# Optimization experiments

Measured on AMD Instinct MI355X. Metric: run time of the kernel, lower is better.

## Reference

```python
import jax, jax.numpy as jnp
import numpy as np

D_MODEL = 768
N_HEADS = 12
D_K = D_MODEL // N_HEADS

def setup_inputs() -> dict:
    key = jax.random.key(0)
    ks = jax.random.split(key, 9)
    B, S = 4, 2048
    s = 1.0 / np.sqrt(D_MODEL)
    return {
        "x": jax.random.normal(ks[0], (B, S, D_MODEL), dtype=jnp.float32),
        "Wq": jax.random.normal(ks[1], (D_MODEL, D_MODEL), dtype=jnp.float32) * s,
        "bq": jnp.zeros((D_MODEL,), dtype=jnp.float32),
        "Wk": jax.random.normal(ks[2], (D_MODEL, D_MODEL), dtype=jnp.float32) * s,
        "bk": jnp.zeros((D_MODEL,), dtype=jnp.float32),
        "Wv": jax.random.normal(ks[3], (D_MODEL, D_MODEL), dtype=jnp.float32) * s,
        "bv": jnp.zeros((D_MODEL,), dtype=jnp.float32),
        "Wo": jax.random.normal(ks[4], (D_MODEL, D_MODEL), dtype=jnp.float32) * s,
        "bo": jnp.zeros((D_MODEL,), dtype=jnp.float32),
    }

def reference(x, Wq, bq, Wk, bk, Wv, bv, Wo, bo):
    B, S, _ = x.shape
    # projections (nn.Linear: x @ W^T + b; here weights stored as (in, out) so x @ W + b)
    q = x @ Wq + bq
    k = x @ Wk + bk
    v = x @ Wv + bv
    # split heads -> (B, H, S, d_k)
    q = q.reshape(B, S, N_HEADS, D_K).transpose(0, 2, 1, 3)
    k = k.reshape(B, S, N_HEADS, D_K).transpose(0, 2, 1, 3)
    v = v.reshape(B, S, N_HEADS, D_K).transpose(0, 2, 1, 3)
    scores = jnp.einsum('bhqd,bhkd->bhqk', q, k) / jnp.sqrt(jnp.float32(D_K))
    causal = jnp.tril(jnp.ones((S, S), dtype=bool))  # True = keep
    scores = jnp.where(causal, scores, jnp.finfo(scores.dtype).min)
    weights = jax.nn.softmax(scores, axis=-1)  # dropout is identity in eval
    out = jnp.einsum('bhqk,bhkd->bhqd', weights, v)
    out = out.transpose(0, 2, 1, 3).reshape(B, S, D_MODEL)
    return out @ Wo + bo
```

## Files before the change

### kernel.cpp

```cpp
#include <hip/hip_runtime.h>
#include <hip/hip_bf16.h>

#define DM    768
#define HEADS 12
#define DK    64
#define SEQ   2048
#define BATCH 4
#define NE    ((size_t)BATCH * SEQ * DM)
#define KT    12
#define BRICK 8192

typedef short v8s __attribute__((ext_vector_type(8)));
typedef float v4f __attribute__((ext_vector_type(4)));

#define LDS_PTR(p) ((__attribute__((address_space(3))) unsigned int*)(p))
#define GLB_PTR(p) ((const __attribute__((address_space(1))) unsigned int*)(p))

__device__ __forceinline__ unsigned short f2bf(float f) {
    union { float f; unsigned u; } v; v.f = f;
    unsigned r = (v.u + 0x7FFFu + ((v.u >> 16) & 1u)) >> 16;
    return (unsigned short)r;
}
__device__ __forceinline__ unsigned pk2(float a, float b) {
    union { float f; unsigned u; } x, y; x.f = a; y.f = b;
    return (x.u >> 16) | (y.u & 0xFFFF0000u);
}
__device__ __forceinline__ unsigned pk2r(float a, float b) {
    return (unsigned)f2bf(a) | ((unsigned)f2bf(b) << 16);
}
__device__ __forceinline__ float fexp2(float x) {
#if __has_builtin(__builtin_amdgcn_exp2f)
    return __builtin_amdgcn_exp2f(x);
#else
    return __expf(x * 0.69314718056f);
#endif
}

#define QSCALE 0.18033688011112042f

__global__ __launch_bounds__(256)
void cvt_x_kernel(const float* __restrict__ x, unsigned short* __restrict__ xb) {
    const size_t p = ((size_t)blockIdx.x * 256 + threadIdx.x) * 8;
    const int m = (int)(p / DM);
    const int k = (int)(p % DM);
    const float4 a = *(const float4*)(x + p);
    const float4 b = *(const float4*)(x + p + 4);
    v8s o;
    o[0] = (short)f2bf(a.x); o[1] = (short)f2bf(a.y);
    o[2] = (short)f2bf(a.z); o[3] = (short)f2bf(a.w);
    o[4] = (short)f2bf(b.x); o[5] = (short)f2bf(b.y);
    o[6] = (short)f2bf(b.z); o[7] = (short)f2bf(b.w);
    const size_t dst = ((size_t)(m >> 7) * KT + (k >> 6)) * BRICK + (size_t)(m & 127) * 64 + (k & 63);
    *(v8s*)(xb + dst) = o;
}

__global__ __launch_bounds__(256)
void cvt_w_kernel(const float* __restrict__ W0, const float* __restrict__ W1,
                  const float* __restrict__ W2, const float* __restrict__ W3,
                  unsigned short* __restrict__ wt) {
    __shared__ unsigned short T[64][72];
    const int z = blockIdx.z;
    const float* W = (z == 0) ? W0 : (z == 1) ? W1 : (z == 2) ? W2 : W3;
    const float scale = (z == 0) ? QSCALE : 1.0f;
    const int k0 = blockIdx.x * 64, n0 = blockIdx.y * 64;
    const int t = threadIdx.x;
    {
        const int kr = t >> 2;
        const int ns = (t & 3) * 16;
        #pragma unroll
        for (int j = 0; j < 4; ++j) {
            const float4 v = *(const float4*)(W + (size_t)(k0 + kr) * DM + n0 + ns + j * 4);
            T[ns + j * 4 + 0][kr] = f2bf(v.x * scale);
            T[ns + j * 4 + 1][kr] = f2bf(v.y * scale);
            T[ns + j * 4 + 2][kr] = f2bf(v.z * scale);
            T[ns + j * 4 + 3][kr] = f2bf(v.w * scale);
        }
    }
    __syncthreads();
    {
        unsigned short* dst = wt + (size_t)z * DM * DM +
            ((size_t)(n0 >> 7) * KT + (k0 >> 6)) * BRICK + (size_t)(n0 & 64) * 64;
        const int n = t >> 2;
        const int ks = (t & 3) * 16;
        #pragma unroll
        for (int j = 0; j < 2; ++j)
            *(v8s*)(dst + (size_t)n * 64 + ks + j * 8) = *(const v8s*)&T[n][ks + j * 8];
    }
}

__global__ __launch_bounds__(256)
void gemm_qkv_kernel(const unsigned short* __restrict__ xb, const unsigned short* __restrict__ wtbuf,
                     const float* __restrict__ bq, const float* __restrict__ bk,
                     const float* __restrict__ bv,
                     unsigned short* __restrict__ qb, unsigned short* __restrict__ kb,
                     unsigned short* __restrict__ vtb) {
    __shared__ unsigned short smem[32768];
    const int idx = blockIdx.x;
    const int xcd = idx & 7, g = idx >> 3;
    const int mb = xcd + 8 * (g & 7);
    const int yb = g >> 3;
    const int z = yb / 6;
    const int N0 = (yb % 6) * 128;
    const float* bias = (z == 0) ? bq : (z == 1) ? bk : bv;
    const float bscale = (z == 0) ? QSCALE : 1.0f;

    const int t = threadIdx.x;
    const int w = t >> 6, lane = t & 63, quad = lane >> 4, l15 = lane & 15;
    const int wm = w >> 1, wn = w & 1;
    const int M0 = mb * 128;

    const unsigned short* gA = xb + (size_t)mb * (KT * BRICK);
    const unsigned short* gB = wtbuf + (size_t)yb * (KT * BRICK);

    const int r8 = lane >> 3;
    const int c8 = (lane & 7) ^ r8;
    const int goff = r8 * 64 + c8 * 8;
    const int rl = l15 & 7, rh = l15 >> 3;

    v4f acc[4][4];
    #pragma unroll
    for (int i = 0; i < 4; ++i)
        #pragma unroll
        for (int j = 0; j < 4; ++j) acc[i][j] = (v4f){0, 0, 0, 0};

    #pragma unroll
    for (int u = 0; u < 4; ++u) {
        const int win = w * 4 + u;
        __builtin_amdgcn_global_load_lds(GLB_PTR(gA + win * 512 + goff), LDS_PTR(smem + win * 512), 16, 0, 0);
        __builtin_amdgcn_global_load_lds(GLB_PTR(gB + win * 512 + goff), LDS_PTR(smem + 16384 + win * 512), 16, 0, 0);
    }
    __syncthreads();

    for (int kt = 0; kt < KT; ++kt) {
        const int cur = kt & 1;
        if (kt + 1 < KT) {
            const unsigned short* ta = gA + (kt + 1) * BRICK;
            const unsigned short* tb = gB + (kt + 1) * BRICK;
            const int nb = (1 - cur) * 8192;
            #pragma unroll
            for (int u = 0; u < 4; ++u) {
                const int win = w * 4 + u;
                __builtin_amdgcn_global_load_lds(GLB_PTR(ta + win * 512 + goff), LDS_PTR(smem + nb + win * 512), 16, 0, 0);
                __builtin_amdgcn_global_load_lds(GLB_PTR(tb + win * 512 + goff), LDS_PTR(smem + 16384 + nb + win * 512), 16, 0, 0);
            }
        }
        const unsigned short* As = smem + cur * 8192;
        const unsigned short* Bs = smem + 16384 + cur * 8192;
        #pragma unroll
        for (int kc = 0; kc < 2; ++kc) {
            const int cs = ((kc << 2) | quad) ^ rl;
            v8s a[4], b[4];
            #pragma unroll
            for (int i = 0; i < 4; ++i)
                a[i] = *(const v8s*)&As[(wm * 8 + i * 2 + rh) * 512 + rl * 64 + cs * 8];
            #pragma unroll
            for (int j = 0; j < 4; ++j)
                b[j] = *(const v8s*)&Bs[(wn * 8 + j * 2 + rh) * 512 + rl * 64 + cs * 8];
            #pragma unroll
            for (int i = 0; i < 4; ++i)
                #pragma unroll
                for (int j = 0; j < 4; ++j)
                    acc[i][j] = __builtin_amdgcn_mfma_f32_16x16x32_bf16(a[i], b[j], acc[i][j], 0, 0, 0);
        }
        __syncthreads();
    }

    const int b_ = M0 >> 11;
    const int sidx0 = M0 & 2047;
    const int h0 = N0 >> 6;

    if (z < 2) {
        unsigned short* outp = (z == 0) ? qb : kb;
        #pragma unroll
        for (int j = 0; j < 4; ++j) {
            const int n = N0 + wn * 64 + j * 16 + l15;
            const int h = n >> 6, d = n & 63;
            const float bv_ = bias[n] * bscale;
            #pragma unroll
            for (int i = 0; i < 4; ++i)
                #pragma unroll
                for (int r = 0; r < 4; ++r) {
                    const int sidx = sidx0 + wm * 64 + i * 16 + quad * 4 + r;
                    outp[(((size_t)(b_ * HEADS + h) * SEQ + sidx) << 6) + d] = f2bf(acc[i][j][r] + bv_);
                }
        }
    } else {
        unsigned short* Ts = smem;
        #pragma unroll
        for (int p = 0; p < 2; ++p) {
            __syncthreads();
            if (wm == p) {
                #pragma unroll
                for (int j = 0; j < 4; ++j) {
                    const int dloc = wn * 64 + j * 16 + l15;
                    const float bv_ = bias[N0 + dloc];
                    #pragma unroll
                    for (int i = 0; i < 4; ++i)
                        #pragma unroll
                        for (int r = 0; r < 4; ++r)
                            Ts[dloc * 72 + i * 16 + quad * 4 + r] = f2bf(acc[i][j][r] + bv_);
                }
            }
            __syncthreads();
            const int dloc = t >> 1, ms = (t & 1) * 32;
            const int h = h0 + (dloc >> 6), d = dloc & 63;
            unsigned short* dst = vtb + (((size_t)(b_ * HEADS + h) * DK + d) << 11) + sidx0 + p * 64 + ms;
            #pragma unroll
            for (int jj = 0; jj < 4; ++jj)
                *(v8s*)(dst + jj * 8) = *(const v8s*)&Ts[dloc * 72 + ms + jj * 8];
        }
    }
}

__global__ __launch_bounds__(256)
void gemm_out_kernel(const unsigned short* __restrict__ ob, const unsigned short* __restrict__ wto,
                     const float* __restrict__ bias, float* __restrict__ out) {
    __shared__ unsigned short smem[32768];
    const int idx = blockIdx.x;
    const int xcd = idx & 7, g = idx >> 3;
    const int mb = xcd + 8 * (g & 7);
    const int nb = g >> 3;
    const int t = threadIdx.x;
    const int w = t >> 6, lane = t & 63, quad = lane >> 4, l15 = lane & 15;
    const int wm = w >> 1, wn = w & 1;
    const int M0 = mb * 128;
    const int N0 = nb * 128;

    const unsigned short* gA = ob + (size_t)mb * (KT * BRICK);
    const unsigned short* gB = wto + (size_t)nb * (KT * BRICK);

    const int r8 = lane >> 3;
    const int c8 = (lane & 7) ^ r8;
    const int goff = r8 * 64 + c8 * 8;
    const int rl = l15 & 7, rh = l15 >> 3;

    v4f acc[4][4];
    #pragma unroll
    for (int i = 0; i < 4; ++i)
        #pragma unroll
        for (int j = 0; j < 4; ++j) acc[i][j] = (v4f){0, 0, 0, 0};

    #pragma unroll
    for (int u = 0; u < 4; ++u) {
        const int win = w * 4 + u;
        __builtin_amdgcn_global_load_lds(GLB_PTR(gA + win * 512 + goff), LDS_PTR(smem + win * 512), 16, 0, 0);
        __builtin_amdgcn_global_load_lds(GLB_PTR(gB + win * 512 + goff), LDS_PTR(smem + 16384 + win * 512), 16, 0, 0);
    }
    __syncthreads();

    for (int kt = 0; kt < KT; ++kt) {
        const int cur = kt & 1;
        if (kt + 1 < KT) {
            const unsigned short* ta = gA + (kt + 1) * BRICK;
            const unsigned short* tb = gB + (kt + 1) * BRICK;
            const int nxt = (1 - cur) * 8192;
            #pragma unroll
            for (int u = 0; u < 4; ++u) {
                const int win = w * 4 + u;
                __builtin_amdgcn_global_load_lds(GLB_PTR(ta + win * 512 + goff), LDS_PTR(smem + nxt + win * 512), 16, 0, 0);
                __builtin_amdgcn_global_load_lds(GLB_PTR(tb + win * 512 + goff), LDS_PTR(smem + 16384 + nxt + win * 512), 16, 0, 0);
            }
        }
        const unsigned short* As = smem + cur * 8192;
        const unsigned short* Bs = smem + 16384 + cur * 8192;
        #pragma unroll
        for (int kc = 0; kc < 2; ++kc) {
            const int cs = ((kc << 2) | quad) ^ rl;
            v8s a[4], b[4];
            #pragma unroll
            for (int i = 0; i < 4; ++i)
                a[i] = *(const v8s*)&As[(wm * 8 + i * 2 + rh) * 512 + rl * 64 + cs * 8];
            #pragma unroll
            for (int j = 0; j < 4; ++j)
                b[j] = *(const v8s*)&Bs[(wn * 8 + j * 2 + rh) * 512 + rl * 64 + cs * 8];
            #pragma unroll
            for (int i = 0; i < 4; ++i)
                #pragma unroll
                for (int j = 0; j < 4; ++j)
                    acc[i][j] = __builtin_amdgcn_mfma_f32_16x16x32_bf16(a[i], b[j], acc[i][j], 0, 0, 0);
        }
        __syncthreads();
    }

    #pragma unroll
    for (int j = 0; j < 4; ++j) {
        const int n = N0 + wn * 64 + j * 16 + l15;
        const float bv_ = bias[n];
        #pragma unroll
        for (int i = 0; i < 4; ++i)
            #pragma unroll
            for (int r = 0; r < 4; ++r) {
                const int m = M0 + wm * 64 + i * 16 + quad * 4 + r;
                out[(size_t)m * DM + n] = acc[i][j][r] + bv_;
            }
    }
}

__global__ __launch_bounds__(256, 3)
void attn_kernel(const unsigned short* __restrict__ Q, const unsigned short* __restrict__ K,
                 const unsigned short* __restrict__ VT, unsigned short* __restrict__ O) {
    __shared__ unsigned short Kb[2][64][72];
    __shared__ unsigned short Vb[2][64][72];
    __shared__ unsigned short Ps[4][16][72];
    const int t = threadIdx.x;
    const int w = t >> 6, lane = t & 63, quad = lane >> 4, l15 = lane & 15;

    const int idx = blockIdx.x;
    const int xcd = idx & 7;
    const int j   = idx >> 3;
    const int bh  = xcd + 8 * (j >> 4);
    const int s   = j & 15;
    const int sA  = s, sB = 31 - s;
    const int q0A = sA * 64, q0B = sB * 64;
    const int nkt = sB + 1;
    const size_t kvbase = (size_t)bh * SEQ * DK;

    v8s qfA[2], qfB[2];
    #pragma unroll
    for (int c = 0; c < 2; ++c) {
        qfA[c] = *(const v8s*)(Q + kvbase + (size_t)(q0A + w * 16 + l15) * DK + c * 32 + quad * 8);
        qfB[c] = *(const v8s*)(Q + kvbase + (size_t)(q0B + w * 16 + l15) * DK + c * 32 + quad * 8);
    }

    v4f oA[4], oB[4];
    #pragma unroll
    for (int nf = 0; nf < 4; ++nf) { oA[nf] = (v4f){0,0,0,0}; oB[nf] = (v4f){0,0,0,0}; }
    float lsA = 0.f, lsB = 0.f;

    const int srow = t >> 3;
    const int scol = (t & 7) * 8;

    v8s kr0 = *(const v8s*)(K  + kvbase + (size_t)srow * DK + scol);
    v8s kr1 = *(const v8s*)(K  + kvbase + (size_t)(srow + 32) * DK + scol);
    v8s vr0 = *(const v8s*)(VT + kvbase + ((size_t)srow << 11) + scol);
    v8s vr1 = *(const v8s*)(VT + kvbase + ((size_t)(srow + 32) << 11) + scol);
    *(v8s*)&Kb[0][srow][scol]      = kr0;
    *(v8s*)&Kb[0][srow + 32][scol] = kr1;
    *(v8s*)&Vb[0][srow][scol]      = vr0;
    *(v8s*)&Vb[0][srow + 32][scol] = vr1;
    __syncthreads();

    const int qA = q0A + w * 16 + l15;
    const int qB = q0B + w * 16 + l15;

    for (int kt = 0; kt < nkt; ++kt) {
        const int k0 = kt * 64;
        const int cur = kt & 1;
        if (kt + 1 < nkt) {
            const int kn = k0 + 64;
            kr0 = *(const v8s*)(K  + kvbase + (size_t)(kn + srow) * DK + scol);
            kr1 = *(const v8s*)(K  + kvbase + (size_t)(kn + srow + 32) * DK + scol);
            vr0 = *(const v8s*)(VT + kvbase + ((size_t)srow << 11) + kn + scol);
            vr1 = *(const v8s*)(VT + kvbase + ((size_t)(srow + 32) << 11) + kn + scol);
        }

        const bool actA = (kt <= sA);

        v4f scB[4], scA[4];
        #pragma unroll
        for (int s4 = 0; s4 < 4; ++s4) { scB[s4] = (v4f){0,0,0,0}; scA[s4] = (v4f){0,0,0,0}; }
        #pragma unroll
        for (int c = 0; c < 2; ++c)
            #pragma unroll
            for (int s4 = 0; s4 < 4; ++s4) {
                const v8s kf = *(const v8s*)&Kb[cur][s4 * 16 + l15][c * 32 + quad * 8];
                scB[s4] = __builtin_amdgcn_mfma_f32_16x16x32_bf16(kf, qfB[c], scB[s4], 0, 0, 0);
                if (actA)
                    scA[s4] = __builtin_amdgcn_mfma_f32_16x16x32_bf16(kf, qfA[c], scA[s4], 0, 0, 0);
            }

        {
            const bool msk = (kt == nkt - 1);
            #pragma unroll
            for (int s4 = 0; s4 < 4; ++s4) {
                float p[4];
                #pragma unroll
                for (int r = 0; r < 4; ++r) {
                    const int key = k0 + s4 * 16 + quad * 4 + r;
                    const float e = fexp2(scB[s4][r]);
                    p[r] = (!msk || key <= qB) ? e : 0.f;
                    lsB += p[r];
                }
                uint2 pkv; pkv.x = pk2(p[0], p[1]); pkv.y = pk2(p[2], p[3]);
                *(uint2*)&Ps[w][l15][s4 * 16 + quad * 4] = pkv;
            }
            #pragma unroll
            for (int kc = 0; kc < 2; ++kc) {
                const v8s pf = *(const v8s*)&Ps[w][l15][kc * 32 + quad * 8];
                #pragma unroll
                for (int nf = 0; nf < 4; ++nf) {
                    const v8s vf = *(const v8s*)&Vb[cur][nf * 16 + l15][kc * 32 + quad * 8];
                    oB[nf] = __builtin_amdgcn_mfma_f32_16x16x32_bf16(vf, pf, oB[nf], 0, 0, 0);
                }
            }
        }

        if (actA) {
            const bool msk = (kt == sA);
            #pragma unroll
            for (int s4 = 0; s4 < 4; ++s4) {
                float p[4];
                #pragma unroll
                for (int r = 0; r < 4; ++r) {
                    const int key = k0 + s4 * 16 + quad * 4 + r;
                    const float e = fexp2(scA[s4][r]);
                    p[r] = (!msk || key <= qA) ? e : 0.f;
                    lsA += p[r];
                }
                uint2 pkv; pkv.x = pk2(p[0], p[1]); pkv.y = pk2(p[2], p[3]);
                *(uint2*)&Ps[w][l15][s4 * 16 + quad * 4] = pkv;
            }
            #pragma unroll
            for (int kc = 0; kc < 2; ++kc) {
                const v8s pf = *(const v8s*)&Ps[w][l15][kc * 32 + quad * 8];
                #pragma unroll
                for (int nf = 0; nf < 4; ++nf) {
                    const v8s vf = *(const v8s*)&Vb[cur][nf * 16 + l15][kc * 32 + quad * 8];
                    oA[nf] = __builtin_amdgcn_mfma_f32_16x16x32_bf16(vf, pf, oA[nf], 0, 0, 0);
                }
            }
        }

        if (kt + 1 < nkt) {
            const int nxt = 1 - cur;
            *(v8s*)&Kb[nxt][srow][scol]      = kr0;
            *(v8s*)&Kb[nxt][srow + 32][scol] = kr1;
            *(v8s*)&Vb[nxt][srow][scol]      = vr0;
            *(v8s*)&Vb[nxt][srow + 32][scol] = vr1;
        }
        __syncthreads();
    }

    lsA += __shfl_xor(lsA, 16); lsA += __shfl_xor(lsA, 32);
    lsB += __shfl_xor(lsB, 16); lsB += __shfl_xor(lsB, 32);
    const float invA = 1.f / lsA, invB = 1.f / lsB;

    const int b = bh / HEADS, h = bh % HEADS;
    const size_t brA = ((size_t)(b * 16 + (q0A >> 7)) * KT + h) * BRICK;
    const size_t brB = ((size_t)(b * 16 + (q0B >> 7)) * KT + h) * BRICK;
    const int rowlA = (q0A & 127) + w * 16 + l15;
    const int rowlB = (q0B & 127) + w * 16 + l15;
    #pragma unroll
    for (int nf = 0; nf < 4; ++nf) {
        uint2 a2, b2;
        a2.x = pk2r(oA[nf][0] * invA, oA[nf][1] * invA);
        a2.y = pk2r(oA[nf][2] * invA, oA[nf][3] * invA);
        b2.x = pk2r(oB[nf][0] * invB, oB[nf][1] * invB);
        b2.y = pk2r(oB[nf][2] * invB, oB[nf][3] * invB);
        *(uint2*)(O + brA + (size_t)rowlA * 64 + nf * 16 + quad * 4) = a2;
        *(uint2*)(O + brB + (size_t)rowlB * 64 + nf * 16 + quad * 4) = b2;
    }
}

extern "C" void kernel_launch(void* const* d_in, const int* in_sizes, int n_in,
                              void* d_out, int out_size, void* d_ws, size_t ws_size,
                              hipStream_t stream) {
    const float* x  = (const float*)d_in[0];
    const float* Wq = (const float*)d_in[1];
    const float* bq = (const float*)d_in[2];
    const float* Wk = (const float*)d_in[3];
    const float* bk = (const float*)d_in[4];
    const float* Wv = (const float*)d_in[5];
    const float* bv = (const float*)d_in[6];
    const float* Wo = (const float*)d_in[7];
    const float* bo = (const float*)d_in[8];
    float* out = (float*)d_out;

    unsigned short* xb  = (unsigned short*)d_ws;
    unsigned short* qb  = xb  + NE;
    unsigned short* kb  = qb  + NE;
    unsigned short* vtb = kb  + NE;
    unsigned short* wt  = vtb + NE;
    unsigned short* ob  = xb;

    cvt_x_kernel<<<dim3(NE / (8 * 256)), 256, 0, stream>>>(x, xb);
    cvt_w_kernel<<<dim3(12, 12, 4), 256, 0, stream>>>(Wq, Wk, Wv, Wo, wt);
    gemm_qkv_kernel<<<dim3(1152), 256, 0, stream>>>(xb, wt, bq, bk, bv, qb, kb, vtb);
    attn_kernel<<<dim3(768), 256, 0, stream>>>(qb, kb, vtb, ob);
    gemm_out_kernel<<<dim3(384), 256, 0, stream>>>(ob, wt + (size_t)3 * DM * DM, bo, out);
}
```

Before: 212.9 us.

## Keep softmax probabilities in registers and feed PV via 16x16x16 MFMA

Removes the per-wave LDS round trip for the probability tile. The score MFMA output layout (4 consecutive keys per lane) is fed directly as the B operand of a 16x16x16 bf16 MFMA, so the exp'd scores are packed in registers with v_perm. The causal mask is also split into an unmasked fast path for non-diagonal tiles, and the A and B query blocks now share each V fragment load. The trade-off is twice as many, smaller MFMAs for PV, which have lower per-instruction throughput, plus extra live registers for pA/pB.

```diff
diff --git a/kernel.cpp b/kernel.cpp
--- a/kernel.cpp
+++ b/kernel.cpp
@@ -11,6 +11,7 @@
 #define BRICK 8192
 
 typedef short v8s __attribute__((ext_vector_type(8)));
+typedef short v4s __attribute__((ext_vector_type(4)));
 typedef float v4f __attribute__((ext_vector_type(4)));
 
 #define LDS_PTR(p) ((__attribute__((address_space(3))) unsigned int*)(p))
@@ -20,10 +21,6 @@
     union { float f; unsigned u; } v; v.f = f;
     unsigned r = (v.u + 0x7FFFu + ((v.u >> 16) & 1u)) >> 16;
     return (unsigned short)r;
-}
-__device__ __forceinline__ unsigned pk2(float a, float b) {
-    union { float f; unsigned u; } x, y; x.f = a; y.f = b;
-    return (x.u >> 16) | (y.u & 0xFFFF0000u);
 }
 __device__ __forceinline__ unsigned pk2r(float a, float b) {
     return (unsigned)f2bf(a) | ((unsigned)f2bf(b) << 16);
@@ -33,6 +30,18 @@
     return __builtin_amdgcn_exp2f(x);
 #else
     return __expf(x * 0.69314718056f);
+#endif
+}
+__device__ __forceinline__ unsigned permpk(float a, float b) {
+    union { float f; unsigned u; } x, y; x.f = a; y.f = b;
+    return __builtin_amdgcn_perm(y.u, x.u, 0x07060302u);
+}
+__device__ __forceinline__ v4f mfma16x16x16(v4s a, v4s b, v4f c) {
+#if __has_builtin(__builtin_amdgcn_mfma_f32_16x16x16bf16_1k)
+    return __builtin_amdgcn_mfma_f32_16x16x16bf16_1k(a, b, c, 0, 0, 0);
+#else
+    asm volatile("v_mfma_f32_16x16x16_bf16 %0, %1, %2, %0" : "+v"(c) : "v"(a), "v"(b));
+    return c;
 #endif
 }
 
@@ -301,7 +310,6 @@
                  const unsigned short* __restrict__ VT, unsigned short* __restrict__ O) {
     __shared__ unsigned short Kb[2][64][72];
     __shared__ unsigned short Vb[2][64][72];
-    __shared__ unsigned short Ps[4][16][72];
     const int t = threadIdx.x;
     const int w = t >> 6, lane = t & 63, quad = lane >> 4, l15 = lane & 15;
 
@@ -324,7 +332,7 @@
 
     v4f oA[4], oB[4];
     #pragma unroll
-    for (int nf = 0; nf < 4; ++nf) { oA[nf] = (v4f){0,0,0,0}; oB[nf] = (v4f){0,0,0,0}; }
+    for (int df = 0; df < 4; ++df) { oA[df] = (v4f){0,0,0,0}; oB[df] = (v4f){0,0,0,0}; }
     float lsA = 0.f, lsB = 0.f;
 
     const int srow = t >> 3;
@@ -342,6 +350,7 @@
 
     const int qA = q0A + w * 16 + l15;
     const int qB = q0B + w * 16 + l15;
+    const int kqbase = quad * 4;
 
     for (int kt = 0; kt < nkt; ++kt) {
         const int k0 = kt * 64;
@@ -369,55 +378,63 @@
                     scA[s4] = __builtin_amdgcn_mfma_f32_16x16x32_bf16(kf, qfA[c], scA[s4], 0, 0, 0);
             }
 
-        {
-            const bool msk = (kt == nkt - 1);
+        uint2 pB[4], pA[4];
+        if (kt < nkt - 1) {
+            #pragma unroll
+            for (int s4 = 0; s4 < 4; ++s4) {
+                const float p0 = fexp2(scB[s4][0]), p1 = fexp2(scB[s4][1]);
+                const float p2 = fexp2(scB[s4][2]), p3 = fexp2(scB[s4][3]);
+                lsB += (p0 + p1) + (p2 + p3);
+                pB[s4].x = permpk(p0, p1); pB[s4].y = permpk(p2, p3);
+            }
+        } else {
             #pragma unroll
             for (int s4 = 0; s4 < 4; ++s4) {
                 float p[4];
                 #pragma unroll
                 for (int r = 0; r < 4; ++r) {
-                    const int key = k0 + s4 * 16 + quad * 4 + r;
+                    const int key = k0 + s4 * 16 + kqbase + r;
                     const float e = fexp2(scB[s4][r]);
-                    p[r] = (!msk || key <= qB) ? e : 0.f;
+                    p[r] = (key <= qB) ? e : 0.f;
                     lsB += p[r];
                 }
-                uint2 pkv; pkv.x = pk2(p[0], p[1]); pkv.y = pk2(p[2], p[3]);
-                *(uint2*)&Ps[w][l15][s4 * 16 + quad * 4] = pkv;
-            }
-            #pragma unroll
-            for (int kc = 0; kc < 2; ++kc) {
-                const v8s pf = *(const v8s*)&Ps[w][l15][kc * 32 + quad * 8];
-                #pragma unroll
-                for (int nf = 0; nf < 4; ++nf) {
-                    const v8s vf = *(const v8s*)&Vb[cur][nf * 16 + l15][kc * 32 + quad * 8];
-                    oB[nf] = __builtin_amdgcn_mfma_f32_16x16x32_bf16(vf, pf, oB[nf], 0, 0, 0);
+                pB[s4].x = permpk(p[0], p[1]); pB[s4].y = permpk(p[2], p[3]);
+            }
+        }
+        if (actA) {
+            if (kt < sA) {
+                #pragma unroll
+                for (int s4 = 0; s4 < 4; ++s4) {
+                    const float p0 = fexp2(scA[s4][0]), p1 = fexp2(scA[s4][1]);
+                    const float p2 = fexp2(scA[s4][2]), p3 = fexp2(scA[s4][3]);
+                    lsA += (p0 + p1) + (p2 + p3);
+                    pA[s4].x = permpk(p0, p1); pA[s4].y = permpk(p2, p3);
                 }
-            }
-        }
-
-        if (actA) {
-            const bool msk = (kt == sA);
-            #pragma unroll
-            for (int s4 = 0; s4 < 4; ++s4) {
-                float p[4];
-                #pragma unroll
-                for (int r = 0; r < 4; ++r) {
-                    const int key = k0 + s4 * 16 + quad * 4 + r;
-                    const float e = fexp2(scA[s4][r]);
-                    p[r] = (!msk || key <= qA) ? e : 0.f;
-                    lsA += p[r];
+            } else {
+                #pragma unroll
+                for (int s4 = 0; s4 < 4; ++s4) {
+                    float p[4];
+                    #pragma unroll
+                    for (int r = 0; r < 4; ++r) {
+                        const int key = k0 + s4 * 16 + kqbase + r;
+                        const float e = fexp2(scA[s4][r]);
+                        p[r] = (key <= qA) ? e : 0.f;
+                        lsA += p[r];
+                    }
+                    pA[s4].x = permpk(p[0], p[1]); pA[s4].y = permpk(p[2], p[3]);
                 }
-                uint2 pkv; pkv.x = pk2(p[0], p[1]); pkv.y = pk2(p[2], p[3]);
-                *(uint2*)&Ps[w][l15][s4 * 16 + quad * 4] = pkv;
-            }
-            #pragma unroll
-            for (int kc = 0; kc < 2; ++kc) {
-                const v8s pf = *(const v8s*)&Ps[w][l15][kc * 32 + quad * 8];
-                #pragma unroll
-                for (int nf = 0; nf < 4; ++nf) {
-                    const v8s vf = *(const v8s*)&Vb[cur][nf * 16 + l15][kc * 32 + quad * 8];
-                    oA[nf] = __builtin_amdgcn_mfma_f32_16x16x32_bf16(vf, pf, oA[nf], 0, 0, 0);
-                }
+            }
+        }
+
+        #pragma unroll
+        for (int s4 = 0; s4 < 4; ++s4) {
+            const v4s pbB = *(const v4s*)&pB[s4];
+            const v4s pbA = *(const v4s*)&pA[s4];
+            #pragma unroll
+            for (int df = 0; df < 4; ++df) {
+                const v4s vf = *(const v4s*)&Vb[cur][df * 16 + l15][s4 * 16 + kqbase];
+                oB[df] = mfma16x16x16(vf, pbB, oB[df]);
+                if (actA) oA[df] = mfma16x16x16(vf, pbA, oA[df]);
             }
         }
 
@@ -441,14 +458,14 @@
     const int rowlA = (q0A & 127) + w * 16 + l15;
     const int rowlB = (q0B & 127) + w * 16 + l15;
     #pragma unroll
-    for (int nf = 0; nf < 4; ++nf) {
+    for (int df = 0; df < 4; ++df) {
         uint2 a2, b2;
-        a2.x = pk2r(oA[nf][0] * invA, oA[nf][1] * invA);
-        a2.y = pk2r(oA[nf][2] * invA, oA[nf][3] * invA);
-        b2.x = pk2r(oB[nf][0] * invB, oB[nf][1] * invB);
-        b2.y = pk2r(oB[nf][2] * invB, oB[nf][3] * invB);
-        *(uint2*)(O + brA + (size_t)rowlA * 64 + nf * 16 + quad * 4) = a2;
-        *(uint2*)(O + brB + (size_t)rowlB * 64 + nf * 16 + quad * 4) = b2;
+        a2.x = pk2r(oA[df][0] * invA, oA[df][1] * invA);
+        a2.y = pk2r(oA[df][2] * invA, oA[df][3] * invA);
+        b2.x = pk2r(oB[df][0] * invB, oB[df][1] * invB);
+        b2.y = pk2r(oB[df][2] * invB, oB[df][3] * invB);
+        *(uint2*)(O + brA + (size_t)rowlA * 64 + df * 16 + quad * 4) = a2;
+        *(uint2*)(O + brB + (size_t)rowlB * 64 + df * 16 + quad * 4) = b2;
     }
 }
 
```

Measured after the change: 226.1 us. 6.2% more time.
